# Kernel optimization log

Hardware: AMD Instinct MI355X
Metric: run time of the kernel (lower is better)

The kernel has to match this reference:

```python
import jax, jax.numpy as jnp
import numpy as np

D = 2048
N = 16384
E = 8
THRESHOLD = 0.5


def setup_inputs() -> dict:
    key = jax.random.key(0)
    ks = jax.random.split(key, 6)
    x = jax.random.normal(ks[0], (N, D), dtype=jnp.float32)
    # pretrained weight + truncated SVD basis (frozen in original module)
    W_np = np.asarray(jax.random.normal(ks[1], (D, D), dtype=jnp.float32))
    U, S, Vt = np.linalg.svd(W_np, full_matrices=False)
    k = int((np.cumsum(S) < THRESHOLD * S.sum()).sum())  # energy-threshold rank
    U_k = jnp.asarray(U[:, :k])
    V_k = jnp.asarray(Vt.T[:, :k])  # torch.svd returns V, not V^T
    W = jnp.asarray(W_np)
    lambda_k = jax.random.normal(ks[2], (E, k), dtype=jnp.float32)
    v = jnp.zeros((D,), dtype=jnp.float32)
    W_g1 = jax.random.normal(ks[3], (k, 1), dtype=jnp.float32)
    W_g2 = jax.random.normal(ks[4], (1, E), dtype=jnp.float32)
    return {"x": x, "W": W, "U_k": U_k, "V_k": V_k, "lambda_k": lambda_k,
            "v": v, "W_g1": W_g1, "W_g2": W_g2}


def reference(x, W, U_k, V_k, lambda_k, v, W_g1, W_g2):
    # Routing: g = softmax((x @ U_k) @ W_g1 @ W_g2)  -> [N, E]
    xu = x @ U_k                                   # [N, k] (shared with delta path)
    g = jax.nn.softmax((xu @ W_g1) @ W_g2, axis=-1)
    # sum_i g_i * (x @ (W + U diag(lam_i) V^T))
    #   = (x@W) * sum_i g_i  +  ((x@U) * (g @ lam)) @ V^T   (low-rank factored)
    base = x @ W                                   # [N, D], computed once
    coef = g @ lambda_k                            # [N, k]
    out = base * jnp.sum(g, axis=-1, keepdims=True) + (xu * coef) @ V_k.T
    return out * (1.0 + v)
```

## Files before the change

### kernel.cpp

```cpp
#include <hip/hip_runtime.h>
#include <hip/hip_bf16.h>

#define D_DIM 2048
#define E_DIM 8

typedef __attribute__((ext_vector_type(8))) short short8;
typedef __attribute__((ext_vector_type(4))) float f32x4;

__device__ __forceinline__ unsigned short f2bf(float f) {
  union { float f; unsigned int u; } v; v.f = f;
  unsigned int u = v.u;
  u += 0x7FFFu + ((u >> 16) & 1u);
  return (unsigned short)(u >> 16);
}

__device__ __forceinline__ void async_copy16(const void* g, void* l) {
  __builtin_amdgcn_global_load_lds((const __attribute__((address_space(1))) void*)g,
                                   (__attribute__((address_space(3))) void*)l,
                                   16, 0, 0);
}

__global__ void k_cvt_bf16(const float* __restrict__ in,
                           unsigned short* __restrict__ out, long long n) {
  long long i = ((long long)blockIdx.x * blockDim.x + threadIdx.x) * 8;
  const long long stride = (long long)gridDim.x * blockDim.x * 8;
  for (; i < n; i += stride) {
    float4 a = *(const float4*)(in + i);
    float4 b = *(const float4*)(in + i + 4);
    short8 r;
    r[0] = (short)f2bf(a.x); r[1] = (short)f2bf(a.y);
    r[2] = (short)f2bf(a.z); r[3] = (short)f2bf(a.w);
    r[4] = (short)f2bf(b.x); r[5] = (short)f2bf(b.y);
    r[6] = (short)f2bf(b.z); r[7] = (short)f2bf(b.w);
    *(short8*)(out + i) = r;
  }
}

__global__ void k_transpose_bf16(const float* __restrict__ in, int in_rows, int in_cols,
                                 int in_ld, unsigned short* __restrict__ out, int out_rows) {
  __shared__ float tile[32][33];
  const int tx = threadIdx.x;
  const int ty = threadIdx.y;
  const int c = blockIdx.x * 32 + tx;
  #pragma unroll
  for (int i = 0; i < 4; ++i) {
    const int r = blockIdx.y * 32 + ty + i * 8;
    float vv = 0.0f;
    if (r < in_rows && c < in_cols) vv = in[(size_t)r * in_ld + c];
    tile[ty + i * 8][tx] = vv;
  }
  __syncthreads();
  const int oc = blockIdx.y * 32 + tx;
  #pragma unroll
  for (int i = 0; i < 4; ++i) {
    const int orow = blockIdx.x * 32 + ty + i * 8;
    if (orow < out_rows && oc < in_rows)
      out[(size_t)orow * in_rows + oc] = f2bf(tile[tx][ty + i * 8]);
  }
}

__global__ void k_pad_bf16(const float* __restrict__ in, unsigned short* __restrict__ out,
                           int rows, int cols, int cols_pad) {
  long long idx = (long long)blockIdx.x * blockDim.x + threadIdx.x;
  const long long total = (long long)rows * cols_pad;
  const long long stride = (long long)gridDim.x * blockDim.x;
  for (; idx < total; idx += stride) {
    const int r = (int)(idx / cols_pad);
    const int c = (int)(idx % cols_pad);
    out[idx] = (c < cols) ? f2bf(in[(size_t)r * cols + c]) : (unsigned short)0;
  }
}

__global__ void k_route(const float* __restrict__ xu, int k, int k_pad,
                        const float* __restrict__ Wg1, const float* __restrict__ Wg2,
                        const float* __restrict__ lam,
                        unsigned short* __restrict__ A2, float* __restrict__ rowscale,
                        int Nrows) {
  const int w = threadIdx.x >> 6;
  const int lane = threadIdx.x & 63;
  const int row = blockIdx.x * 4 + w;
  if (row >= Nrows) return;
  const float* xr = xu + (size_t)row * k_pad;
  float s = 0.0f;
  for (int kk = lane; kk < k; kk += 64) s += xr[kk] * Wg1[kk];
  #pragma unroll
  for (int off = 32; off; off >>= 1) s += __shfl_xor(s, off);
  float lg[E_DIM];
  float mx = -INFINITY;
  #pragma unroll
  for (int e = 0; e < E_DIM; ++e) { lg[e] = s * Wg2[e]; mx = fmaxf(mx, lg[e]); }
  float Z = 0.0f;
  #pragma unroll
  for (int e = 0; e < E_DIM; ++e) { lg[e] = expf(lg[e] - mx); Z += lg[e]; }
  float g[E_DIM]; float gsum = 0.0f;
  #pragma unroll
  for (int e = 0; e < E_DIM; ++e) { g[e] = lg[e] / Z; gsum += g[e]; }
  const float inv = 1.0f / gsum;
  if (lane == 0) rowscale[row] = gsum;
  unsigned short* arow = A2 + (size_t)row * k_pad;
  for (int kk = lane; kk < k_pad; kk += 64) {
    if (kk < k) {
      float c = 0.0f;
      #pragma unroll
      for (int e = 0; e < E_DIM; ++e) c += g[e] * lam[(size_t)e * k + kk];
      arow[kk] = f2bf(xr[kk] * (c * inv));
    } else {
      arow[kk] = 0;
    }
  }
}

template<int EPI>
__global__ __launch_bounds__(256, 2) void k_gemm(
    const unsigned short* __restrict__ A0, int lda0,
    const unsigned short* __restrict__ A1, int lda1,
    const unsigned short* __restrict__ B0, int ldb0,
    const unsigned short* __restrict__ B1, int ldb1,
    int ka0, int Ktot,
    float* __restrict__ Cout, int ldc,
    const float* __restrict__ rowscale, const float* __restrict__ vcol) {
  __shared__ unsigned short As[128 * 32];
  __shared__ unsigned short Bs[128 * 32];
  const int tid = threadIdx.x;
  const int lane = tid & 63;
  const int w = tid >> 6;
  const int brow = blockIdx.x * 128;
  const int bcol = blockIdx.y * 128;

  f32x4 acc[4][4];
  #pragma unroll
  for (int m = 0; m < 4; ++m)
    #pragma unroll
    for (int n2 = 0; n2 < 4; ++n2)
      #pragma unroll
      for (int j = 0; j < 4; ++j) acc[m][n2][j] = 0.0f;

  const int srow = lane >> 2;
  const int scol = (lane & 3) * 8;
  const int wr = (w >> 1) * 64;
  const int wc = (w & 1) * 64;
  const int nkt = Ktot >> 5;

  for (int kt = 0; kt < nkt; ++kt) {
    const int k0 = kt * 32;
    const unsigned short* Ab; int ldA; int kA;
    const unsigned short* Bb; int ldB; int kB;
    if (k0 < ka0) { Ab = A0; ldA = lda0; kA = k0;       Bb = B0; ldB = ldb0; kB = k0; }
    else          { Ab = A1; ldA = lda1; kA = k0 - ka0; Bb = B1; ldB = ldb1; kB = k0 - ka0; }
    __syncthreads();
    #pragma unroll
    for (int p = 0; p < 2; ++p) {
      const int c = p * 4 + w;
      const int row = c * 16 + srow;
      async_copy16(Ab + (size_t)(brow + row) * ldA + kA + scol, (void*)(As + c * 512));
      async_copy16(Bb + (size_t)(bcol + row) * ldB + kB + scol, (void*)(Bs + c * 512));
    }
    __syncthreads();
    short8 av[4], bv[4];
    #pragma unroll
    for (int m = 0; m < 4; ++m)
      av[m] = *(const short8*)(As + (wr + m * 16 + (lane & 15)) * 32 + (lane >> 4) * 8);
    #pragma unroll
    for (int n2 = 0; n2 < 4; ++n2)
      bv[n2] = *(const short8*)(Bs + (wc + n2 * 16 + (lane & 15)) * 32 + (lane >> 4) * 8);
    #pragma unroll
    for (int m = 0; m < 4; ++m)
      #pragma unroll
      for (int n2 = 0; n2 < 4; ++n2)
        acc[m][n2] = __builtin_amdgcn_mfma_f32_16x16x32_bf16(av[m], bv[n2], acc[m][n2], 0, 0, 0);
  }

  #pragma unroll
  for (int m = 0; m < 4; ++m) {
    #pragma unroll
    for (int n2 = 0; n2 < 4; ++n2) {
      const int col = bcol + wc + n2 * 16 + (lane & 15);
      float cs = 1.0f;
      if (EPI == 1) cs = 1.0f + vcol[col];
      #pragma unroll
      for (int j = 0; j < 4; ++j) {
        const int row = brow + wr + m * 16 + (lane >> 4) * 4 + j;
        float val = acc[m][n2][j];
        if (EPI == 1) val *= rowscale[row] * cs;
        Cout[(size_t)row * ldc + col] = val;
      }
    }
  }
}

template<int EPI>
__global__ __launch_bounds__(512, 2) void k_gemm256(
    const unsigned short* __restrict__ A0, int lda0,
    const unsigned short* __restrict__ A1, int lda1,
    const unsigned short* __restrict__ B0, int ldb0,
    const unsigned short* __restrict__ B1, int ldb1,
    int ka0, int Ktot, int gridM,
    float* __restrict__ Cout, int ldc,
    const float* __restrict__ rowscale, const float* __restrict__ vcol) {
  __shared__ unsigned short lds[4 * 16384];
  const int tid = threadIdx.x;
  const int lane = tid & 63;
  const int w = tid >> 6;
  const int wm = w >> 2;
  const int wn = w & 3;

  int bid = blockIdx.x;
  const int cpx = gridDim.x >> 3;
  bid = (bid & 7) * cpx + (bid >> 3);
  const int bx = bid % gridM;
  const int by = bid / gridM;
  const long long brow = (long long)bx * 256;
  const long long bcol = (long long)by * 256;

  const int c0 = w * 2;
  const int sr0 = lane >> 2;
  const int sj  = lane & 3;

  auto stage = [&](int tt, const unsigned short* P, long long ldP, int kbase,
                   long long rbase, int breg) {
    unsigned short* dst = lds + (tt & 3) * 16384 + breg * 8192;
    #pragma unroll
    for (int c = 0; c < 2; ++c) {
      const int chunk = c0 + c;
      const int lrow = chunk * 16 + sr0;
      const int jj = sj ^ ((lrow >> 1) & 3);
      const unsigned short* src = P + (rbase + lrow) * ldP + kbase + jj * 8;
      async_copy16(src, (void*)(dst + chunk * 512));
    }
  };

  const int NT = Ktot >> 5;

  auto segA = [&](int tt, const unsigned short*& P, long long& ld, int& kb) {
    const int k0 = tt * 32;
    if (k0 < ka0) { P = A0; ld = lda0; kb = k0; }
    else          { P = A1; ld = lda1; kb = k0 - ka0; }
  };
  auto segB = [&](int tt, const unsigned short*& P, long long& ld, int& kb) {
    const int k0 = tt * 32;
    if (k0 < ka0) { P = B0; ld = ldb0; kb = k0; }
    else          { P = B1; ld = ldb1; kb = k0 - ka0; }
  };

  for (int p = 0; p < 3; ++p) {
    const unsigned short* PA; long long ldA; int kA; segA(p, PA, ldA, kA);
    const unsigned short* PB; long long ldB; int kB; segB(p, PB, ldB, kB);
    stage(p, PA, ldA, kA, brow, 0);
    stage(p, PB, ldB, kB, bcol, 1);
  }
  asm volatile("s_waitcnt vmcnt(8)" ::: "memory");
  __builtin_amdgcn_s_barrier();

  f32x4 acc[8][4];
  #pragma unroll
  for (int m = 0; m < 8; ++m)
    #pragma unroll
    for (int n = 0; n < 4; ++n)
      #pragma unroll
      for (int j = 0; j < 4; ++j) acc[m][n][j] = 0.0f;

  const int l15 = lane & 15;
  const int jhi = lane >> 4;

  for (int t = 0; t < NT; ++t) {
    const unsigned short* Areg = lds + (t & 3) * 16384;
    const unsigned short* Breg = Areg + 8192;
    short8 av[8], bv[2];

    #pragma unroll
    for (int m = 0; m < 8; ++m) {
      const int row = wm * 128 + m * 16 + l15;
      const int jj = jhi ^ ((row >> 1) & 3);
      av[m] = *(const short8*)(Areg + row * 32 + jj * 8);
    }
    #pragma unroll
    for (int n = 0; n < 2; ++n) {
      const int row = wn * 64 + n * 16 + l15;
      const int jj = jhi ^ ((row >> 1) & 3);
      bv[n] = *(const short8*)(Breg + row * 32 + jj * 8);
    }
    if (t + 3 < NT) {
      const unsigned short* PA; long long ldA; int kA; segA(t + 3, PA, ldA, kA);
      stage(t + 3, PA, ldA, kA, brow, 0);
    }
    __builtin_amdgcn_s_barrier();
    __builtin_amdgcn_s_setprio(1);
    #pragma unroll
    for (int m = 0; m < 8; ++m)
      #pragma unroll
      for (int n = 0; n < 2; ++n)
        acc[m][n] = __builtin_amdgcn_mfma_f32_16x16x32_bf16(av[m], bv[n], acc[m][n], 0, 0, 0);
    __builtin_amdgcn_s_setprio(0);
    __builtin_amdgcn_s_barrier();

    #pragma unroll
    for (int n = 0; n < 2; ++n) {
      const int row = wn * 64 + 32 + n * 16 + l15;
      const int jj = jhi ^ ((row >> 1) & 3);
      bv[n] = *(const short8*)(Breg + row * 32 + jj * 8);
    }
    if (t + 3 < NT) {
      const unsigned short* PB; long long ldB; int kB; segB(t + 3, PB, ldB, kB);
      stage(t + 3, PB, ldB, kB, bcol, 1);
    }
    __builtin_amdgcn_s_barrier();
    __builtin_amdgcn_s_setprio(1);
    #pragma unroll
    for (int m = 0; m < 8; ++m)
      #pragma unroll
      for (int n = 0; n < 2; ++n)
        acc[m][2 + n] = __builtin_amdgcn_mfma_f32_16x16x32_bf16(av[m], bv[n], acc[m][2 + n], 0, 0, 0);
    __builtin_amdgcn_s_setprio(0);
    if (t + 3 < NT)      asm volatile("s_waitcnt vmcnt(8)" ::: "memory");
    else if (t + 2 < NT) asm volatile("s_waitcnt vmcnt(4)" ::: "memory");
    else if (t + 1 < NT) asm volatile("s_waitcnt vmcnt(0)" ::: "memory");
    __builtin_amdgcn_s_barrier();
  }

  #pragma unroll
  for (int m = 0; m < 8; ++m) {
    #pragma unroll
    for (int n = 0; n < 4; ++n) {
      const long long col = bcol + wn * 64 + n * 16 + l15;
      float cs = 1.0f;
      if (EPI == 1) cs = 1.0f + vcol[col];
      #pragma unroll
      for (int j = 0; j < 4; ++j) {
        const long long row = brow + wm * 128 + m * 16 + jhi * 4 + j;
        float val = acc[m][n][j];
        if (EPI == 1) val *= rowscale[row] * cs;
        Cout[row * ldc + col] = val;
      }
    }
  }
}

extern "C" void kernel_launch(void* const* d_in, const int* in_sizes, int n_in,
                              void* d_out, int out_size, void* d_ws, size_t ws_size,
                              hipStream_t stream) {
  const float* x   = (const float*)d_in[0];
  const float* W   = (const float*)d_in[1];
  const float* U   = (const float*)d_in[2];
  const float* V   = (const float*)d_in[3];
  const float* lam = (const float*)d_in[4];
  const float* v   = (const float*)d_in[5];
  const float* Wg1 = (const float*)d_in[6];
  const float* Wg2 = (const float*)d_in[7];
  float* out = (float*)d_out;

  const int N = in_sizes[0] / D_DIM;
  const int k = in_sizes[2] / D_DIM;
  const int k_pad = (k + 127) & ~127;

  char* ws = (char*)d_ws;
  size_t off = 0;
  auto alloc = [&](size_t bytes) -> void* {
    void* p = ws + off;
    off += (bytes + 255) & ~(size_t)255;
    return p;
  };
  unsigned short* xb  = (unsigned short*)alloc((size_t)N * D_DIM * 2);
  unsigned short* Wt  = (unsigned short*)alloc((size_t)D_DIM * D_DIM * 2);
  unsigned short* Ukt = (unsigned short*)alloc((size_t)k_pad * D_DIM * 2);
  unsigned short* Vb  = (unsigned short*)alloc((size_t)D_DIM * k_pad * 2);
  float*          xu  = (float*)alloc((size_t)N * k_pad * 4);
  unsigned short* A2  = (unsigned short*)alloc((size_t)N * k_pad * 2);
  float*          rs  = (float*)alloc((size_t)N * 4);
  if (off > ws_size) return;

  k_cvt_bf16<<<2048, 256, 0, stream>>>(x, xb, (long long)N * D_DIM);
  k_transpose_bf16<<<dim3(D_DIM / 32, D_DIM / 32), dim3(32, 8), 0, stream>>>(
      W, D_DIM, D_DIM, D_DIM, Wt, D_DIM);
  k_transpose_bf16<<<dim3(k_pad / 32, D_DIM / 32), dim3(32, 8), 0, stream>>>(
      U, D_DIM, k, k, Ukt, k_pad);
  k_pad_bf16<<<512, 256, 0, stream>>>(V, Vb, D_DIM, k, k_pad);

  k_gemm<0><<<dim3(N / 128, k_pad / 128), 256, 0, stream>>>(
      xb, D_DIM, nullptr, 0,
      Ukt, D_DIM, nullptr, 0,
      D_DIM, D_DIM,
      xu, k_pad, nullptr, nullptr);

  k_route<<<N / 4, 256, 0, stream>>>(xu, k, k_pad, Wg1, Wg2, lam, A2, rs, N);

  const int gridM = N / 256;
  const int gridN = D_DIM / 256;
  k_gemm256<1><<<gridM * gridN, 512, 0, stream>>>(
      xb, D_DIM, A2, k_pad,
      Wt, D_DIM, Vb, k_pad,
      D_DIM, D_DIM + k_pad, gridM,
      out, D_DIM, rs, v);
}
```

Before: 348.9 us.

## Pipeline the xu GEMM with async multi-buffering and single-phase main loop

```diff
diff --git a/kernel.cpp b/kernel.cpp
--- a/kernel.cpp
+++ b/kernel.cpp
@@ -110,79 +110,89 @@
   }
 }
 
-template<int EPI>
-__global__ __launch_bounds__(256, 2) void k_gemm(
-    const unsigned short* __restrict__ A0, int lda0,
-    const unsigned short* __restrict__ A1, int lda1,
-    const unsigned short* __restrict__ B0, int ldb0,
-    const unsigned short* __restrict__ B1, int ldb1,
-    int ka0, int Ktot,
-    float* __restrict__ Cout, int ldc,
-    const float* __restrict__ rowscale, const float* __restrict__ vcol) {
-  __shared__ unsigned short As[128 * 32];
-  __shared__ unsigned short Bs[128 * 32];
+__global__ __launch_bounds__(256, 2) void k_gemm128(
+    const unsigned short* __restrict__ A, long long lda,
+    const unsigned short* __restrict__ B, long long ldb,
+    int Ktot, float* __restrict__ Cout, int ldc) {
+  __shared__ unsigned short lds[4 * 8192];
   const int tid = threadIdx.x;
   const int lane = tid & 63;
   const int w = tid >> 6;
-  const int brow = blockIdx.x * 128;
-  const int bcol = blockIdx.y * 128;
+  const long long brow = (long long)blockIdx.x * 128;
+  const long long bcol = (long long)blockIdx.y * 128;
+  const int c0 = w * 2;
+  const int sr0 = lane >> 2;
+  const int sj  = lane & 3;
+
+  auto stage = [&](int tt, const unsigned short* P, long long ldP, long long rbase, int breg) {
+    unsigned short* dst = lds + (tt & 3) * 8192 + breg * 4096;
+    #pragma unroll
+    for (int c = 0; c < 2; ++c) {
+      const int chunk = c0 + c;
+      const int lrow = chunk * 16 + sr0;
+      const int jj = sj ^ ((lrow >> 1) & 3);
+      async_copy16(P + (rbase + lrow) * ldP + (long long)tt * 32 + jj * 8,
+                   (void*)(dst + chunk * 512));
+    }
+  };
+
+  const int NT = Ktot >> 5;
+  for (int p = 0; p < 3; ++p) { stage(p, A, lda, brow, 0); stage(p, B, ldb, bcol, 1); }
+  asm volatile("s_waitcnt vmcnt(8)" ::: "memory");
+  __builtin_amdgcn_s_barrier();
 
   f32x4 acc[4][4];
   #pragma unroll
   for (int m = 0; m < 4; ++m)
     #pragma unroll
-    for (int n2 = 0; n2 < 4; ++n2)
-      #pragma unroll
-      for (int j = 0; j < 4; ++j) acc[m][n2][j] = 0.0f;
-
-  const int srow = lane >> 2;
-  const int scol = (lane & 3) * 8;
+    for (int n = 0; n < 4; ++n)
+      #pragma unroll
+      for (int j = 0; j < 4; ++j) acc[m][n][j] = 0.0f;
+
+  const int l15 = lane & 15;
+  const int jhi = lane >> 4;
   const int wr = (w >> 1) * 64;
   const int wc = (w & 1) * 64;
-  const int nkt = Ktot >> 5;
-
-  for (int kt = 0; kt < nkt; ++kt) {
-    const int k0 = kt * 32;
-    const unsigned short* Ab; int ldA; int kA;
-    const unsigned short* Bb; int ldB; int kB;
-    if (k0 < ka0) { Ab = A0; ldA = lda0; kA = k0;       Bb = B0; ldB = ldb0; kB = k0; }
-    else          { Ab = A1; ldA = lda1; kA = k0 - ka0; Bb = B1; ldB = ldb1; kB = k0 - ka0; }
-    __syncthreads();
-    #pragma unroll
-    for (int p = 0; p < 2; ++p) {
-      const int c = p * 4 + w;
-      const int row = c * 16 + srow;
-      async_copy16(Ab + (size_t)(brow + row) * ldA + kA + scol, (void*)(As + c * 512));
-      async_copy16(Bb + (size_t)(bcol + row) * ldB + kB + scol, (void*)(Bs + c * 512));
-    }
-    __syncthreads();
+
+  for (int t = 0; t < NT; ++t) {
+    const unsigned short* Areg = lds + (t & 3) * 8192;
+    const unsigned short* Breg = Areg + 4096;
+    if (t + 3 < NT) { stage(t + 3, A, lda, brow, 0); stage(t + 3, B, ldb, bcol, 1); }
     short8 av[4], bv[4];
     #pragma unroll
+    for (int m = 0; m < 4; ++m) {
+      const int row = wr + m * 16 + l15;
+      const int jj = jhi ^ ((row >> 1) & 3);
+      av[m] = *(const short8*)(Areg + row * 32 + jj * 8);
+    }
+    #pragma unroll
+    for (int n = 0; n < 4; ++n) {
+      const int row = wc + n * 16 + l15;
+      const int jj = jhi ^ ((row >> 1) & 3);
+      bv[n] = *(const short8*)(Breg + row * 32 + jj * 8);
+    }
+    __builtin_amdgcn_s_setprio(1);
+    #pragma unroll
     for (int m = 0; m < 4; ++m)
-      av[m] = *(const short8*)(As + (wr + m * 16 + (lane & 15)) * 32 + (lane >> 4) * 8);
-    #pragma unroll
-    for (int n2 = 0; n2 < 4; ++n2)
-      bv[n2] = *(const short8*)(Bs + (wc + n2 * 16 + (lane & 15)) * 32 + (lane >> 4) * 8);
-    #pragma unroll
-    for (int m = 0; m < 4; ++m)
-      #pragma unroll
-      for (int n2 = 0; n2 < 4; ++n2)
-        acc[m][n2] = __builtin_amdgcn_mfma_f32_16x16x32_bf16(av[m], bv[n2], acc[m][n2], 0, 0, 0);
+      #pragma unroll
+      for (int n = 0; n < 4; ++n)
+        acc[m][n] = __builtin_amdgcn_mfma_f32_16x16x32_bf16(av[m], bv[n], acc[m][n], 0, 0, 0);
+    __builtin_amdgcn_s_setprio(0);
+    if (t + 3 < NT)      asm volatile("s_waitcnt vmcnt(8)" ::: "memory");
+    else if (t + 2 < NT) asm volatile("s_waitcnt vmcnt(4)" ::: "memory");
+    else if (t + 1 < NT) asm volatile("s_waitcnt vmcnt(0)" ::: "memory");
+    __builtin_amdgcn_s_barrier();
   }
 
   #pragma unroll
   for (int m = 0; m < 4; ++m) {
     #pragma unroll
-    for (int n2 = 0; n2 < 4; ++n2) {
-      const int col = bcol + wc + n2 * 16 + (lane & 15);
-      float cs = 1.0f;
-      if (EPI == 1) cs = 1.0f + vcol[col];
+    for (int n = 0; n < 4; ++n) {
+      const long long col = bcol + wc + n * 16 + l15;
       #pragma unroll
       for (int j = 0; j < 4; ++j) {
-        const int row = brow + wr + m * 16 + (lane >> 4) * 4 + j;
-        float val = acc[m][n2][j];
-        if (EPI == 1) val *= rowscale[row] * cs;
-        Cout[(size_t)row * ldc + col] = val;
+        const long long row = brow + wr + m * 16 + jhi * 4 + j;
+        Cout[row * ldc + col] = acc[m][n][j];
       }
     }
   }
@@ -265,8 +275,15 @@
   for (int t = 0; t < NT; ++t) {
     const unsigned short* Areg = lds + (t & 3) * 16384;
     const unsigned short* Breg = Areg + 8192;
-    short8 av[8], bv[2];
-
+
+    if (t + 3 < NT) {
+      const unsigned short* PA; long long ldA; int kA; segA(t + 3, PA, ldA, kA);
+      stage(t + 3, PA, ldA, kA, brow, 0);
+      const unsigned short* PB; long long ldB; int kB; segB(t + 3, PB, ldB, kB);
+      stage(t + 3, PB, ldB, kB, bcol, 1);
+    }
+
+    short8 av[8], bv[4];
     #pragma unroll
     for (int m = 0; m < 8; ++m) {
       const int row = wm * 128 + m * 16 + l15;
@@ -274,43 +291,20 @@
       av[m] = *(const short8*)(Areg + row * 32 + jj * 8);
     }
     #pragma unroll
-    for (int n = 0; n < 2; ++n) {
+    for (int n = 0; n < 4; ++n) {
       const int row = wn * 64 + n * 16 + l15;
       const int jj = jhi ^ ((row >> 1) & 3);
       bv[n] = *(const short8*)(Breg + row * 32 + jj * 8);
     }
-    if (t + 3 < NT) {
-      const unsigned short* PA; long long ldA; int kA; segA(t + 3, PA, ldA, kA);
-      stage(t + 3, PA, ldA, kA, brow, 0);
-    }
-    __builtin_amdgcn_s_barrier();
+
     __builtin_amdgcn_s_setprio(1);
     #pragma unroll
     for (int m = 0; m < 8; ++m)
       #pragma unroll
-      for (int n = 0; n < 2; ++n)
+      for (int n = 0; n < 4; ++n)
         acc[m][n] = __builtin_amdgcn_mfma_f32_16x16x32_bf16(av[m], bv[n], acc[m][n], 0, 0, 0);
     __builtin_amdgcn_s_setprio(0);
-    __builtin_amdgcn_s_barrier();
-
-    #pragma unroll
-    for (int n = 0; n < 2; ++n) {
-      const int row = wn * 64 + 32 + n * 16 + l15;
-      const int jj = jhi ^ ((row >> 1) & 3);
-      bv[n] = *(const short8*)(Breg + row * 32 + jj * 8);
-    }
-    if (t + 3 < NT) {
-      const unsigned short* PB; long long ldB; int kB; segB(t + 3, PB, ldB, kB);
-      stage(t + 3, PB, ldB, kB, bcol, 1);
-    }
-    __builtin_amdgcn_s_barrier();
-    __builtin_amdgcn_s_setprio(1);
-    #pragma unroll
-    for (int m = 0; m < 8; ++m)
-      #pragma unroll
-      for (int n = 0; n < 2; ++n)
-        acc[m][2 + n] = __builtin_amdgcn_mfma_f32_16x16x32_bf16(av[m], bv[n], acc[m][2 + n], 0, 0, 0);
-    __builtin_amdgcn_s_setprio(0);
+
     if (t + 3 < NT)      asm volatile("s_waitcnt vmcnt(8)" ::: "memory");
     else if (t + 2 < NT) asm volatile("s_waitcnt vmcnt(4)" ::: "memory");
     else if (t + 1 < NT) asm volatile("s_waitcnt vmcnt(0)" ::: "memory");
@@ -375,11 +369,8 @@
       U, D_DIM, k, k, Ukt, k_pad);
   k_pad_bf16<<<512, 256, 0, stream>>>(V, Vb, D_DIM, k, k_pad);
 
-  k_gemm<0><<<dim3(N / 128, k_pad / 128), 256, 0, stream>>>(
-      xb, D_DIM, nullptr, 0,
-      Ukt, D_DIM, nullptr, 0,
-      D_DIM, D_DIM,
-      xu, k_pad, nullptr, nullptr);
+  k_gemm128<<<dim3(N / 128, k_pad / 128), 256, 0, stream>>>(
+      xb, D_DIM, Ukt, D_DIM, D_DIM, xu, k_pad);
 
   k_route<<<N / 4, 256, 0, stream>>>(xu, k, k_pad, Wg1, Wg2, lam, A2, rs, N);
 
```

New measurement: 347.5 us. No clear change (-0.4%).
